# Optimization experiments

Hardware: AMD Instinct MI355X
Metric: run time of the kernel (lower is better)

The kernel has to match this reference:

```python
import jax, jax.numpy as jnp
import numpy as np
import math

B, N, C = 1, 2048, 256
H, CH = 8, 32
PQ, PV = 8, 12
CZ = 32
BQ, BK = 32, 128
NB = N // BQ
PAD = (BK - BQ) // 2
INF = 1e8
EPS = 1e-8

_KIDX = np.arange(NB)[:, None] * BQ + np.arange(BK)[None, :] - PAD
_KVALID = (_KIDX >= 0) & (_KIDX < N)
_KIDX_C = np.clip(_KIDX, 0, N - 1)


def _quat_to_rot(q):
    q = q / jnp.linalg.norm(q, axis=-1, keepdims=True)
    w, x, y, z = q[..., 0], q[..., 1], q[..., 2], q[..., 3]
    return jnp.stack([
        jnp.stack([1 - 2 * (y * y + z * z), 2 * (x * y - w * z), 2 * (x * z + w * y)], -1),
        jnp.stack([2 * (x * y + w * z), 1 - 2 * (x * x + z * z), 2 * (y * z - w * x)], -1),
        jnp.stack([2 * (x * z - w * y), 2 * (y * z + w * x), 1 - 2 * (x * x + y * y)], -1)], -2)


def _to_queries(x):
    # [B, N, ...] -> [B, NB, BQ, ...]
    return x.reshape((B, NB, BQ) + x.shape[2:])


def _to_keys(x):
    # [B, N, ...] -> [B, NB, BK, ...] zero-padded sliding key windows
    g = x[:, _KIDX_C]
    v = jnp.asarray(_KVALID, x.dtype).reshape((1, NB, BK) + (1,) * (x.ndim - 2))
    return g * v


def _ln(x):
    m = x.mean(-1, keepdims=True)
    var = x.var(-1, keepdims=True)
    return (x - m) / jnp.sqrt(var + 1e-5)


def setup_inputs():
    key = jax.random.key(0)
    ks = jax.random.split(key, 16)
    p = 0.02
    return {
        's': jax.random.normal(ks[0], (B, N, C), jnp.float32),
        'cond': jax.random.normal(ks[1], (B, N, C), jnp.float32),
        'z': jax.random.normal(ks[2], (B, NB, BQ, BK, CZ), jnp.float32),
        'trans': jax.random.normal(ks[3], (B, N, 3), jnp.float32),
        'rots': _quat_to_rot(jax.random.normal(ks[4], (B, N, 4), jnp.float32)),
        's_mask': jnp.ones((B, N), jnp.float32),
        'Wq': jax.random.normal(ks[5], (C, H * CH)) * p,
        'Wk': jax.random.normal(ks[6], (C, H * CH)) * p,
        'Wv': jax.random.normal(ks[7], (C, H * CH)) * p,
        'Wqp': jax.random.normal(ks[8], (C, H * PQ * 3)) * p,
        'Wkvp': jax.random.normal(ks[9], (C, H * (PQ + PV) * 3)) * p,
        'Wb': jax.random.normal(ks[10], (CZ, H)) * p,
        'Wdz': jax.random.normal(ks[11], (CZ, CZ // 4)) * p,
        'head_weights': jnp.full((H,), 0.5413),
        'Wout': jax.random.normal(ks[12], (H * (CZ // 4 + CH + PV * 4), C)) * p,
        'Wg': jax.random.normal(ks[13], (C, C)) * p,
        'bg': jnp.zeros((C,)),
        'Wbeta': jax.random.normal(ks[14], (C, C)) * p,
        'bbeta': jnp.zeros((C,)),
        'g_z': jnp.ones((CZ,)),
        'b_z': jnp.zeros((CZ,)),
    }


def reference(s, cond, z, trans, rots, s_mask, Wq, Wk, Wv, Wqp, Wkvp, Wb, Wdz,
              head_weights, Wout, Wg, bg, Wbeta, bbeta, g_z, b_z):
    # AdaLN on s conditioned on cond; LayerNorm on z
    s = _ln(s) * (cond @ Wg + bg) + (cond @ Wbeta + bbeta)
    z = _ln(z) * g_z + b_z

    q_in = _to_queries(s)            # [B,NB,BQ,C]
    k_in = _to_keys(s)               # [B,NB,BK,C]
    q_t = _to_queries(trans)         # [B,NB,BQ,3]
    q_R = _to_queries(rots)          # [B,NB,BQ,3,3]
    k_t = _to_keys(trans)
    k_R = _to_keys(rots)
    # zero-padded key rotations -> identity
    zero = jnp.all(k_R == 0, axis=(-2, -1))[..., None, None]
    k_R = jnp.where(zero, jnp.eye(3, dtype=k_R.dtype), k_R)

    q = (q_in @ Wq).reshape(B, NB, BQ, H, CH)
    k = (k_in @ Wk).reshape(B, NB, BK, H, CH)
    v = (k_in @ Wv).reshape(B, NB, BK, H, CH)

    q_pts = (q_in @ Wqp).reshape(B, NB, BQ, H * PQ, 3)
    q_pts = jnp.einsum('bnqij,bnqpj->bnqpi', q_R, q_pts) + q_t[..., None, :]
    q_pts = q_pts.reshape(B, NB, BQ, H, PQ, 3)

    kv_pts = (k_in @ Wkvp).reshape(B, NB, BK, H * (PQ + PV), 3)
    kv_pts = jnp.einsum('bnkij,bnkpj->bnkpi', k_R, kv_pts) + k_t[..., None, :]
    kv_pts = kv_pts.reshape(B, NB, BK, H, PQ + PV, 3)
    k_pts, v_pts = kv_pts[..., :PQ, :], kv_pts[..., PQ:, :]

    b = z @ Wb                                    # [B,NB,BQ,BK,H]
    a = jnp.einsum('bnqhc,bnkhc->bnqkh', q, k) * math.sqrt(1.0 / (3 * CH))
    a = a + math.sqrt(1.0 / 3.0) * b

    disp = q_pts[:, :, :, None] - k_pts[:, :, None]   # [B,NB,BQ,BK,H,PQ,3]
    d2 = jnp.sum(disp * disp, axis=-1)                # [B,NB,BQ,BK,H,PQ]
    hw = jax.nn.softplus(head_weights) * math.sqrt(1.0 / (3 * (PQ * 9.0 / 2)))
    pt_att = -0.5 * jnp.sum(d2 * hw[:, None], axis=-1)   # [B,NB,BQ,BK,H]

    m_q = _to_queries(s_mask[..., None])              # [B,NB,BQ,1]
    m_k = _to_keys(s_mask[..., None])                 # [B,NB,BK,1]
    attn_mask = m_q * jnp.swapaxes(m_k, -1, -2)       # [B,NB,BQ,BK]
    attn_mask = INF * (attn_mask - 1.0)

    a = a + pt_att + attn_mask[..., None]
    a = jnp.swapaxes(a, -1, -2)                       # [B,NB,BQ,H,BK]
    a = jax.nn.softmax(a, axis=-1)

    o = jnp.einsum('bnqhk,bnkhc->bnqhc', a, v).reshape(B, NB, BQ, H * CH)
    o_pt = jnp.einsum('bnqhk,bnkhvc->bnqhvc', a, v_pts)      # [B,NB,BQ,H,PV,3]
    o_pt = jnp.einsum('bnqji,bnqhvj->bnqhvi', q_R,
                      o_pt - q_t[:, :, :, None, None, :])     # invert apply
    o_pt_norm = jnp.sqrt(jnp.sum(o_pt ** 2, -1) + EPS).reshape(B, NB, BQ, H * PV)
    o_pt = o_pt.reshape(B, NB, BQ, H * PV * 3)
    pair_z = z @ Wdz                                          # [B,NB,BQ,BK,CZ//4]
    o_pair = jnp.einsum('bnqhk,bnqkc->bnqhc', a, pair_z).reshape(B, NB, BQ, H * (CZ // 4))

    out = jnp.concatenate([o, o_pt, o_pt_norm, o_pair], -1) @ Wout
    return out.reshape(B, N, C)
```

## Files before the change

kernel.cpp:

```cpp
#include <hip/hip_runtime.h>
#include <hip/hip_bf16.h>
#include <math.h>

typedef __hip_bfloat16 bf16;
typedef __attribute__((ext_vector_type(8))) short short8;
typedef __attribute__((ext_vector_type(4))) short short4v;
typedef __attribute__((ext_vector_type(4))) float f32x4;

#define NRES 2048
#define CDIM 256
#define PADK 48
#define POS 1440

static __device__ __forceinline__ float b2f(bf16 x) { return __bfloat162float(x); }
static __device__ __forceinline__ float us2f(short u) {
    return __uint_as_float(((unsigned)(unsigned short)u) << 16);
}
static __device__ __forceinline__ short f2s(float f) {
    bf16 h = __float2bfloat16(f);
    return *reinterpret_cast<short*>(&h);
}
static __device__ __forceinline__ bool flag_f32(const void* smask) {
    return *(const unsigned int*)smask == 0x3F800000u;
}
static __device__ __forceinline__ float dual_load(const void* p, size_t i, bool f32) {
    float vf = ((const float*)p)[f32 ? i : 0];
    float vb = b2f(((const bf16*)p)[f32 ? (size_t)0 : i]);
    return f32 ? vf : vb;
}

struct PrepTable {
    const void* src[8];
    bf16* dst[8];
    int srcN[8];
    int nOff[8];
    int dstStride[8];
    float scl[8];
    int tileOff[9];
    const void* s;
    const void* cond;
    bf16* condb;
    bf16* xnb;
    const void* rots;
    const void* trans;
    float* RT;
    const void* z;
    const void* Wb;
    const void* Wdz;
    const void* g_z;
    const void* b_z;
    bf16* Bzb;
    bf16* PZb;
};
__global__ __launch_bounds__(256) void k_prep(PrepTable tb, const void* __restrict__ smask) {
    __shared__ float tile[32][33];
    __shared__ float ls[8][CDIM];
    __shared__ float mrs[8][2];
    __shared__ float wb[32][8], wdz[32][8], gz[32], bz[32];
    bool f32 = flag_f32(smask);
    int b = blockIdx.x;
    int t = threadIdx.x;
    if (b < tb.tileOff[8]) {
        int s = 0;
        while (b >= tb.tileOff[s + 1]) ++s;
        int rel = b - tb.tileOff[s];
        int ntTiles = tb.srcN[s] >> 5;
        int kt = rel / ntTiles, nt = rel % ntTiles;
        const void* src = tb.src[s];
        int srcN = tb.srcN[s];
        float scl = tb.scl[s];
        int tx = t & 31, ty = t >> 5;
#pragma unroll
        for (int r = 0; r < 4; ++r) {
            int srow = kt * 32 + ty + r * 8;
            int scol = nt * 32 + tx;
            tile[ty + r * 8][tx] = dual_load(src, (size_t)srow * srcN + scol, f32);
        }
        __syncthreads();
        bf16* dst = tb.dst[s];
#pragma unroll
        for (int r = 0; r < 4; ++r) {
            int n = nt * 32 + ty + r * 8 + tb.nOff[s];
            int k = kt * 32 + tx;
            dst[(size_t)n * tb.dstStride[s] + k] = __float2bfloat16(tile[tx][ty + r * 8] * scl);
        }
        return;
    }
    b -= tb.tileOff[8];
    if (b < 256) {
        int i0 = b * 2048;
        for (int i = t; i < 2048; i += 256)
            tb.condb[i0 + i] = __float2bfloat16(dual_load(tb.cond, (size_t)(i0 + i), f32));
        return;
    }
    b -= 256;
    if (b < 256) {
        int r0 = b * 8;
        for (int i = t; i < 8 * CDIM; i += 256) {
            int r = i >> 8, c = i & 255;
            ls[r][c] = dual_load(tb.s, (size_t)(r0 + r) * CDIM + c, f32);
        }
        __syncthreads();
        int wave = t >> 6, lane = t & 63;
        for (int rr = 0; rr < 2; ++rr) {
            int r = wave * 2 + rr;
            float sum = 0.f, sq = 0.f;
            for (int j = lane; j < CDIM; j += 64) { float v = ls[r][j]; sum += v; sq += v * v; }
            for (int off = 32; off; off >>= 1) { sum += __shfl_xor(sum, off); sq += __shfl_xor(sq, off); }
            if (lane == 0) {
                float m = sum / CDIM;
                float var = fmaxf(sq / CDIM - m * m, 0.f);
                mrs[r][0] = m; mrs[r][1] = rsqrtf(var + 1e-5f);
            }
        }
        __syncthreads();
        int c = t;
#pragma unroll
        for (int r = 0; r < 8; ++r)
            tb.xnb[(size_t)(r0 + r) * CDIM + c] = __float2bfloat16((ls[r][c] - mrs[r][0]) * mrs[r][1]);
        return;
    }
    b -= 256;
    if (b < 96) {
        int i = b * 256 + t;
        int row = i / 12, c = i % 12;
        float v = (c < 9) ? dual_load(tb.rots, (size_t)row * 9 + c, f32)
                          : dual_load(tb.trans, (size_t)row * 3 + (c - 9), f32);
        tb.RT[i] = v;
        return;
    }
    b -= 96;
    {
        int j = t >> 3, c = t & 7;
        wb[j][c] = 0.5773502691896258f * dual_load(tb.Wb, t, f32);
        wdz[j][c] = dual_load(tb.Wdz, t, f32);
    }
    if (t < 32) { gz[t] = dual_load(tb.g_z, t, f32); bz[t] = dual_load(tb.b_z, t, f32); }
    __syncthreads();
    size_t r = (size_t)b * 256 + t;
    float zv[32];
    float sum = 0.f, sq = 0.f;
    if (f32) {
        const float4* zp = (const float4*)((const float*)tb.z + r * 32);
#pragma unroll
        for (int j4 = 0; j4 < 8; ++j4) {
            float4 v4 = zp[j4];
            zv[j4 * 4 + 0] = v4.x; zv[j4 * 4 + 1] = v4.y; zv[j4 * 4 + 2] = v4.z; zv[j4 * 4 + 3] = v4.w;
        }
    } else {
        const bf16* zp = (const bf16*)tb.z + r * 32;
#pragma unroll
        for (int j = 0; j < 32; ++j) zv[j] = b2f(zp[j]);
    }
#pragma unroll
    for (int j = 0; j < 32; ++j) { float v = zv[j]; sum += v; sq += v * v; }
    float m = sum / 32.f;
    float var = fmaxf(sq / 32.f - m * m, 0.f);
    float rstd = rsqrtf(var + 1e-5f);
#pragma unroll
    for (int j = 0; j < 32; ++j) zv[j] = (zv[j] - m) * rstd * gz[j] + bz[j];
    float bacc[8], pacc[8];
#pragma unroll
    for (int c = 0; c < 8; ++c) { bacc[c] = 0.f; pacc[c] = 0.f; }
    for (int j = 0; j < 32; ++j) {
        float v = zv[j];
#pragma unroll
        for (int c = 0; c < 8; ++c) { bacc[c] += v * wb[j][c]; pacc[c] += v * wdz[j][c]; }
    }
    int n = (int)(r >> 12);
    int q = (int)(r >> 7) & 31;
    int k = (int)r & 127;
#pragma unroll
    for (int h = 0; h < 8; ++h)
        tb.Bzb[(size_t)n * 32768 + (size_t)h * 4096 + q * 128 + k] = __float2bfloat16(bacc[h]);
#pragma unroll
    for (int c = 0; c < 8; ++c)
        tb.PZb[(((size_t)(n * 32 + q)) * 8 + c) * 128 + k] = __float2bfloat16(pacc[c]);
}

__global__ __launch_bounds__(256) void k_gb(
    const bf16* __restrict__ condb, const bf16* __restrict__ GWt, const bf16* __restrict__ xnb,
    const void* __restrict__ bg, const void* __restrict__ bbeta,
    const void* __restrict__ smask, bf16* __restrict__ SQb)
{
    bool f32 = flag_f32(smask);
    int wid = threadIdx.x >> 6, lane = threadIdx.x & 63;
    int tid = blockIdx.x * 4 + wid;
    int mt = tid >> 4, nt = tid & 15;
    int idx = lane & 15, quad = lane >> 4;
    const bf16* Ap = condb + (size_t)(mt * 16 + idx) * 256 + quad * 8;
    const bf16* B0 = GWt + (size_t)(nt * 16 + idx) * 256 + quad * 8;
    const bf16* B1 = GWt + (size_t)(256 + nt * 16 + idx) * 256 + quad * 8;
    f32x4 a0 = {0,0,0,0}, a1 = {0,0,0,0};
    for (int k = 0; k < 256; k += 32) {
        short8 af = *(const short8*)(Ap + k);
        a0 = __builtin_amdgcn_mfma_f32_16x16x32_bf16(af, *(const short8*)(B0 + k), a0, 0, 0, 0);
        a1 = __builtin_amdgcn_mfma_f32_16x16x32_bf16(af, *(const short8*)(B1 + k), a1, 0, 0, 0);
    }
    int ocol = nt * 16 + idx;
    float bgc = dual_load(bg, ocol, f32), bbc = dual_load(bbeta, ocol, f32);
    int orow = mt * 16 + quad * 4;
#pragma unroll
    for (int r = 0; r < 4; ++r) {
        int row = orow + r;
        float xn = b2f(xnb[(size_t)row * 256 + ocol]);
        SQb[(size_t)row * 256 + ocol] = __float2bfloat16(xn * (a0[r] + bgc) + (a1[r] + bbc));
    }
}

__global__ __launch_bounds__(256) void k_gemm22b(
    const bf16* __restrict__ A, const bf16* __restrict__ Bt, bf16* __restrict__ C,
    int N, int K, int totalWaves)
{
    int wid = threadIdx.x >> 6, lane = threadIdx.x & 63;
    int tid = blockIdx.x * 4 + wid;
    if (tid >= totalWaves) return;
    int tiles_n = N >> 5;
    int mt = tid / tiles_n, nt = tid % tiles_n;
    int idx = lane & 15, quad = lane >> 4;
    const bf16* Ap0 = A + (size_t)(mt * 32 + idx) * K + quad * 8;
    const bf16* Ap1 = Ap0 + (size_t)16 * K;
    const bf16* Bp0 = Bt + (size_t)(nt * 32 + idx) * K + quad * 8;
    const bf16* Bp1 = Bp0 + (size_t)16 * K;
    f32x4 a00 = {0,0,0,0}, a01 = {0,0,0,0}, a10 = {0,0,0,0}, a11 = {0,0,0,0};
    for (int k = 0; k < K; k += 32) {
        short8 af0 = *(const short8*)(Ap0 + k);
        short8 af1 = *(const short8*)(Ap1 + k);
        short8 bf0 = *(const short8*)(Bp0 + k);
        short8 bf1 = *(const short8*)(Bp1 + k);
        a00 = __builtin_amdgcn_mfma_f32_16x16x32_bf16(af0, bf0, a00, 0, 0, 0);
        a01 = __builtin_amdgcn_mfma_f32_16x16x32_bf16(af0, bf1, a01, 0, 0, 0);
        a10 = __builtin_amdgcn_mfma_f32_16x16x32_bf16(af1, bf0, a10, 0, 0, 0);
        a11 = __builtin_amdgcn_mfma_f32_16x16x32_bf16(af1, bf1, a11, 0, 0, 0);
    }
    int orow = mt * 32 + quad * 4;
    int ocol = nt * 32 + idx;
#pragma unroll
    for (int r = 0; r < 4; ++r) {
        C[(size_t)(orow + r) * N + ocol] = __float2bfloat16(a00[r]);
        C[(size_t)(orow + r) * N + ocol + 16] = __float2bfloat16(a01[r]);
        C[(size_t)(orow + r + 16) * N + ocol] = __float2bfloat16(a10[r]);
        C[(size_t)(orow + r + 16) * N + ocol + 16] = __float2bfloat16(a11[r]);
    }
}

__global__ __launch_bounds__(256) void k_attn_out(
    const bf16* __restrict__ POb,
    const bf16* __restrict__ Bzb, const bf16* __restrict__ PZb,
    const float* __restrict__ RT,
    const void* __restrict__ smask, const void* __restrict__ head_weights,
    bf16* __restrict__ CATb)
{
    __shared__ char buf[70016];
    __shared__ float rowq[32], rowk[128], mk[128], mqv[32];
    short* QfS = (short*)buf;
    short* KfS = (short*)(buf + 4608);
    short* VtS = (short*)(buf + 23040);
    short* AsS = (short*)(buf + 44800);
    float* S   = (float*)(buf + 53504);
    float* OPT = (float*)(buf + 53504);
    short* PtsS = (short*)(buf + 44800);
    short* QpS  = (short*)(buf + 62208);

    const int n = blockIdx.x >> 3, h = blockIdx.x & 7;
    const int t = threadIdx.x;
    const bool f32 = flag_f32(smask);
    const int n32 = n * 32;

    float hwv = dual_load(head_weights, h, f32);
    float ptc = -0.5f * log1pf(expf(hwv)) * 0.09622504486493764f;
    float m2ptc = -2.f * ptc;
    const short8 zero8 = {0,0,0,0,0,0,0,0};
    const short4v zero4 = {0,0,0,0};

    if (t < 128) {
        int q = t >> 2, g = t & 3;
        *(short8*)(QfS + q * 72 + g * 8) =
            *(const short8*)(POb + (size_t)(n32 + q) * POS + h * 32 + g * 8);
    }
    for (int i = t; i < 512; i += 256) {
        int k = i >> 2, g = i & 3;
        int kg = n32 + k - PADK;
        short8 v = zero8;
        if (kg >= 0 && kg < NRES)
            v = *(const short8*)(POb + (size_t)kg * POS + 256 + h * 32 + g * 8);
        *(short8*)(KfS + k * 72 + g * 8) = v;
    }
    for (int i = t; i < 512; i += 256) {
        int k = i >> 2, g = i & 3;
        int kg = n32 + k - PADK;
        short8 v = zero8;
        if (kg >= 0 && kg < NRES)
            v = *(const short8*)(POb + (size_t)kg * POS + 512 + h * 32 + g * 8);
#pragma unroll
        for (int j = 0; j < 8; ++j) VtS[(g * 8 + j) * 136 + k] = v[j];
    }
    for (int i = t; i < 1920; i += 256) {
        int k = i / 15, g = i % 15;
        int kg = n32 + k - PADK;
        short4v v = zero4;
        if (kg >= 0 && kg < NRES)
            v = *(const short4v*)(POb + (size_t)kg * POS + 960 + h * 60 + g * 4);
        *(short4v*)(PtsS + k * 68 + g * 4) = v;
    }
    if (t < 192) {
        int q = t / 6, g = t % 6;
        *(short4v*)(QpS + q * 28 + g * 4) =
            *(const short4v*)(POb + (size_t)(n32 + q) * POS + 768 + h * 24 + g * 4);
    }
    for (int i = t; i < 320; i += 256) {
        if (i < 64) { int q = i >> 1, g = i & 1; *(short8*)(QfS + q * 72 + 56 + g * 8) = zero8; }
        else { int j = i - 64; int k = j >> 1, g = j & 1; *(short8*)(KfS + k * 72 + 56 + g * 8) = zero8; }
    }
    for (int i = t; i < 204; i += 256) {
        int r = 68 + i / 17, sg = i % 17;
        *(short8*)(VtS + r * 136 + sg * 8) = zero8;
    }
    __syncthreads();

    {
        int k = t >> 1, half = t & 1;
        int kg = n32 + k - PADK;
        bool valid = (kg >= 0 && kg < NRES);
        if (valid) {
            const float4* rt = (const float4*)(RT + (size_t)kg * 12);
            float4 r0 = rt[0], r1 = rt[1], r2 = rt[2];
            float s2 = 0.f;
            int j0 = half * 10;
#pragma unroll
            for (int jj = 0; jj < 10; ++jj) {
                int j = j0 + jj;
                float x = us2f(PtsS[k * 68 + j * 3 + 0]);
                float y = us2f(PtsS[k * 68 + j * 3 + 1]);
                float z = us2f(PtsS[k * 68 + j * 3 + 2]);
                float p0 = r0.x * x + r0.y * y + r0.z * z + r2.y;
                float p1 = r0.w * x + r1.x * y + r1.y * z + r2.z;
                float p2 = r1.z * x + r1.w * y + r2.x * z + r2.w;
                if (j < 8) {
                    KfS[k * 72 + 32 + j * 3 + 0] = f2s(p0);
                    KfS[k * 72 + 32 + j * 3 + 1] = f2s(p1);
                    KfS[k * 72 + 32 + j * 3 + 2] = f2s(p2);
                    s2 += p0 * p0 + p1 * p1 + p2 * p2;
                } else {
                    int v = j - 8;
                    VtS[(32 + v * 3 + 0) * 136 + k] = f2s(p0);
                    VtS[(32 + v * 3 + 1) * 136 + k] = f2s(p1);
                    VtS[(32 + v * 3 + 2) * 136 + k] = f2s(p2);
                }
            }
            if (half == 0) {
                rowk[k] = ptc * s2;
                mk[k] = dual_load(smask, kg, f32);
            }
        } else {
            if (half == 0) {
                for (int c = 32; c < 56; ++c) KfS[k * 72 + c] = 0;
                for (int x = 32; x < 50; ++x) VtS[x * 136 + k] = 0;
                rowk[k] = 0.f; mk[k] = 0.f;
            } else {
                for (int x = 50; x < 68; ++x) VtS[x * 136 + k] = 0;
            }
        }
    }
    if (t < 32) {
        int q = t;
        int g = n32 + q;
        const float4* rt = (const float4*)(RT + (size_t)g * 12);
        float4 r0 = rt[0], r1 = rt[1], r2 = rt[2];
        mqv[q] = dual_load(smask, g, f32);
        float s2 = 0.f;
#pragma unroll
        for (int p = 0; p < 8; ++p) {
            float x = us2f(QpS[q * 28 + p * 3 + 0]);
            float y = us2f(QpS[q * 28 + p * 3 + 1]);
            float z = us2f(QpS[q * 28 + p * 3 + 2]);
            float p0 = r0.x * x + r0.y * y + r0.z * z + r2.y;
            float p1 = r0.w * x + r1.x * y + r1.y * z + r2.z;
            float p2 = r1.z * x + r1.w * y + r2.x * z + r2.w;
            QfS[q * 72 + 32 + p * 3 + 0] = f2s(m2ptc * p0);
            QfS[q * 72 + 32 + p * 3 + 1] = f2s(m2ptc * p1);
            QfS[q * 72 + 32 + p * 3 + 2] = f2s(m2ptc * p2);
            s2 += p0 * p0 + p1 * p1 + p2 * p2;
        }
        rowq[q] = ptc * s2;
    }
    __syncthreads();

    const int wid = t >> 6, lane = t & 63, idx = lane & 15, quad = lane >> 4;
#pragma unroll
    for (int i = 0; i < 4; ++i) {
        int tt = wid * 4 + i;
        int mt = tt >> 3, nt = tt & 7;
        f32x4 acc = {0.f, 0.f, 0.f, 0.f};
#pragma unroll
        for (int kk = 0; kk < 2; ++kk) {
            short8 af  = *(const short8*)(QfS + (mt * 16 + idx) * 72 + kk * 32 + quad * 8);
            short8 bfv = *(const short8*)(KfS + (nt * 16 + idx) * 72 + kk * 32 + quad * 8);
            acc = __builtin_amdgcn_mfma_f32_16x16x32_bf16(af, bfv, acc, 0, 0, 0);
        }
#pragma unroll
        for (int r = 0; r < 4; ++r) {
            int q = mt * 16 + quad * 4 + r;
            int k = nt * 16 + idx;
            float bz = b2f(Bzb[(size_t)n * 32768 + (size_t)h * 4096 + q * 128 + k]);
            float msk = 1e8f * (mqv[q] * mk[k] - 1.f);
            S[q * 129 + k] = acc[r] + bz + rowq[q] + rowk[k] + msk;
        }
    }
    __syncthreads();

    for (int rr = 0; rr < 8; ++rr) {
        int q = wid * 8 + rr;
        float v0 = S[q * 129 + lane], v1 = S[q * 129 + lane + 64];
        float mx = fmaxf(v0, v1);
        for (int off = 32; off; off >>= 1) mx = fmaxf(mx, __shfl_xor(mx, off));
        float e0 = expf(v0 - mx), e1 = expf(v1 - mx);
        float sm = e0 + e1;
        for (int off = 32; off; off >>= 1) sm += __shfl_xor(sm, off);
        float inv = 1.f / sm;
        AsS[q * 136 + lane] = f2s(e0 * inv);
        AsS[q * 136 + lane + 64] = f2s(e1 * inv);
    }
    __syncthreads();

    {
        int q = t >> 3, c = t & 7;
        const short8* pzp = (const short8*)(PZb + ((size_t)(n32 + q) * 8 + c) * 128);
        const short8* asp = (const short8*)(AsS + q * 136);
        float acc = 0.f;
        for (int k8 = 0; k8 < 16; ++k8) {
            short8 pv = pzp[k8];
            short8 av = asp[k8];
#pragma unroll
            for (int j = 0; j < 8; ++j) acc += us2f(av[j]) * us2f(pv[j]);
        }
        CATb[(size_t)(n32 + q) * 704 + 640 + h * 8 + c] = __float2bfloat16(acc);
    }
#pragma unroll
    for (int i = 0; i < 3; ++i) {
        int tt = wid + i * 4;
        if (tt >= 10) break;
        int mt = tt / 5, nt = tt % 5;
        f32x4 acc = {0.f, 0.f, 0.f, 0.f};
#pragma unroll
        for (int kk = 0; kk < 4; ++kk) {
            short8 af  = *(const short8*)(AsS + (mt * 16 + idx) * 136 + kk * 32 + quad * 8);
            short8 bfv = *(const short8*)(VtS + (nt * 16 + idx) * 136 + kk * 32 + quad * 8);
            acc = __builtin_amdgcn_mfma_f32_16x16x32_bf16(af, bfv, acc, 0, 0, 0);
        }
        int x = nt * 16 + idx;
#pragma unroll
        for (int r = 0; r < 4; ++r) {
            int q = mt * 16 + quad * 4 + r;
            if (x < 32)
                CATb[(size_t)(n32 + q) * 704 + h * 32 + x] = __float2bfloat16(acc[r]);
            else if (x < 68)
                OPT[q * 37 + (x - 32)] = acc[r];
        }
    }
    __syncthreads();

    for (int i = t; i < 384; i += 256) {
        int q = i / 12, v = i % 12;
        int g = n32 + q;
        const float4* rt = (const float4*)(RT + (size_t)g * 12);
        float4 r0 = rt[0], r1 = rt[1], r2 = rt[2];
        float x = OPT[q * 37 + v * 3 + 0] - r2.y;
        float y = OPT[q * 37 + v * 3 + 1] - r2.z;
        float z = OPT[q * 37 + v * 3 + 2] - r2.w;
        float o0 = r0.x * x + r0.w * y + r1.z * z;
        float o1 = r0.y * x + r1.x * y + r1.w * z;
        float o2 = r0.z * x + r1.y * y + r2.x * z;
        size_t cb = (size_t)g * 704;
        CATb[cb + 256 + (h * 12 + v) * 3 + 0] = __float2bfloat16(o0);
        CATb[cb + 256 + (h * 12 + v) * 3 + 1] = __float2bfloat16(o1);
        CATb[cb + 256 + (h * 12 + v) * 3 + 2] = __float2bfloat16(o2);
        CATb[cb + 544 + h * 12 + v] = __float2bfloat16(sqrtf(o0 * o0 + o1 * o1 + o2 * o2 + 1e-8f));
    }
}

__global__ __launch_bounds__(256) void k_gemm(
    const bf16* __restrict__ A, const bf16* __restrict__ Bt, void* __restrict__ Cv,
    int N, int K, int totalTiles, const void* __restrict__ smask)
{
    int wid = threadIdx.x >> 6, lane = threadIdx.x & 63;
    int tid = blockIdx.x * 4 + wid;
    if (tid >= totalTiles) return;
    int tiles_n = N >> 4;
    int mt = tid / tiles_n, nt = tid % tiles_n;
    int idx = lane & 15, quad = lane >> 4;
    const bf16* Ap = A + (size_t)(mt * 16 + idx) * K + quad * 8;
    const bf16* Bp = Bt + (size_t)(nt * 16 + idx) * K + quad * 8;
    f32x4 acc = {0.f, 0.f, 0.f, 0.f};
    for (int k = 0; k < K; k += 32) {
        short8 af = *(const short8*)(Ap + k);
        short8 bfv = *(const short8*)(Bp + k);
        acc = __builtin_amdgcn_mfma_f32_16x16x32_bf16(af, bfv, acc, 0, 0, 0);
    }
    int orow = mt * 16 + quad * 4;
    int ocol = nt * 16 + idx;
    if (flag_f32(smask)) {
        float* C = (float*)Cv;
#pragma unroll
        for (int r = 0; r < 4; ++r) C[(size_t)(orow + r) * N + ocol] = acc[r];
    } else {
        bf16* C = (bf16*)Cv;
#pragma unroll
        for (int r = 0; r < 4; ++r) C[(size_t)(orow + r) * N + ocol] = __float2bfloat16(acc[r]);
    }
}

extern "C" void kernel_launch(void* const* d_in, const int* in_sizes, int n_in,
                              void* d_out, int out_size, void* d_ws, size_t ws_size,
                              hipStream_t stream) {
    const void* s       = d_in[0];
    const void* cond    = d_in[1];
    const void* z       = d_in[2];
    const void* trans   = d_in[3];
    const void* rots    = d_in[4];
    const void* s_mask  = d_in[5];
    const void* Wq      = d_in[6];
    const void* Wk      = d_in[7];
    const void* Wv      = d_in[8];
    const void* Wqp     = d_in[9];
    const void* Wkvp    = d_in[10];
    const void* Wb      = d_in[11];
    const void* Wdz     = d_in[12];
    const void* hweights= d_in[13];
    const void* Wout    = d_in[14];
    const void* Wg      = d_in[15];
    const void* bg      = d_in[16];
    const void* Wbeta   = d_in[17];
    const void* bbeta   = d_in[18];
    const void* g_z     = d_in[19];
    const void* b_z     = d_in[20];

    float* ws = (float*)d_ws;
    bf16* POb   = (bf16*)(ws);
    bf16* Bzb   = (bf16*)(ws + 1474560);
    bf16* PZb   = (bf16*)(ws + 2523136);
    bf16* SQb   = (bf16*)(ws + 3571712);
    bf16* condb = (bf16*)(ws + 3833856);
    bf16* xnb   = (bf16*)(ws + 4096000);
    bf16* CATb  = (bf16*)(ws + 4358144);
    bf16* PWt   = (bf16*)(ws + 5079040);
    bf16* GWt   = (bf16*)(ws + 5263360);
    bf16* FWt   = (bf16*)(ws + 5328896);
    float* RT   = (float*)(ws + 5419008);

    PrepTable tb;
    const float qkscale = 0.10206207261596575f;
    tb.src[0] = Wq;   tb.dst[0] = PWt; tb.srcN[0] = 256; tb.nOff[0] = 0;   tb.dstStride[0] = 256; tb.scl[0] = qkscale;
    tb.src[1] = Wk;   tb.dst[1] = PWt; tb.srcN[1] = 256; tb.nOff[1] = 256; tb.dstStride[1] = 256; tb.scl[1] = 1.f;
    tb.src[2] = Wv;   tb.dst[2] = PWt; tb.srcN[2] = 256; tb.nOff[2] = 512; tb.dstStride[2] = 256; tb.scl[2] = 1.f;
    tb.src[3] = Wqp;  tb.dst[3] = PWt; tb.srcN[3] = 192; tb.nOff[3] = 768; tb.dstStride[3] = 256; tb.scl[3] = 1.f;
    tb.src[4] = Wkvp; tb.dst[4] = PWt; tb.srcN[4] = 480; tb.nOff[4] = 960; tb.dstStride[4] = 256; tb.scl[4] = 1.f;
    tb.src[5] = Wg;   tb.dst[5] = GWt; tb.srcN[5] = 256; tb.nOff[5] = 0;   tb.dstStride[5] = 256; tb.scl[5] = 1.f;
    tb.src[6] = Wbeta;tb.dst[6] = GWt; tb.srcN[6] = 256; tb.nOff[6] = 256; tb.dstStride[6] = 256; tb.scl[6] = 1.f;
    tb.src[7] = Wout; tb.dst[7] = FWt; tb.srcN[7] = 256; tb.nOff[7] = 0;   tb.dstStride[7] = 704; tb.scl[7] = 1.f;
    int tc[8] = {64, 64, 64, 48, 120, 64, 64, 176};
    tb.tileOff[0] = 0;
    for (int i = 0; i < 8; ++i) tb.tileOff[i + 1] = tb.tileOff[i] + tc[i];
    tb.s = s; tb.cond = cond; tb.condb = condb; tb.xnb = xnb;
    tb.rots = rots; tb.trans = trans; tb.RT = RT;
    tb.z = z; tb.Wb = Wb; tb.Wdz = Wdz; tb.g_z = g_z; tb.b_z = b_z;
    tb.Bzb = Bzb; tb.PZb = PZb;

    dim3 blk(256);
    k_prep<<<dim3(2296), blk, 0, stream>>>(tb, s_mask);
    k_gb<<<dim3(512), blk, 0, stream>>>(condb, GWt, xnb, bg, bbeta, s_mask, SQb);
    k_gemm22b<<<dim3(720), blk, 0, stream>>>(SQb, PWt, POb, 1440, 256, 2880);
    k_attn_out<<<dim3(512), blk, 0, stream>>>(POb, Bzb, PZb, RT, s_mask, hweights, CATb);
    k_gemm<<<dim3(512), blk, 0, stream>>>(CATb, FWt, d_out, 256, 704, 2048, s_mask);
}
```

Baseline: 177.5 us.

## Prefetch frames, Bz tile and pair-z into registers/LDS; reorder prep blocks

In the attention kernel, rotation/translation frames and masks are loaded into registers at kernel start, and the per-head Bz bias tile is staged into LDS with vector loads instead of scattered global reads inside the score loop. The PZb rows are loaded into registers before the V MFMA so their latency overlaps it, and the o_pair dot product runs afterwards. In the prep kernel the heavy z-layernorm blocks are moved to the front of the grid so they are scheduled first. This adds about 8.7KB of LDS and 64 registers of short8 per thread, which may reduce occupancy.

```diff
diff --git a/kernel.cpp b/kernel.cpp
--- a/kernel.cpp
+++ b/kernel.cpp
@@ -60,6 +60,56 @@
     bool f32 = flag_f32(smask);
     int b = blockIdx.x;
     int t = threadIdx.x;
+    if (b < 1024) {
+        {
+            int j = t >> 3, c = t & 7;
+            wb[j][c] = 0.5773502691896258f * dual_load(tb.Wb, t, f32);
+            wdz[j][c] = dual_load(tb.Wdz, t, f32);
+        }
+        if (t < 32) { gz[t] = dual_load(tb.g_z, t, f32); bz[t] = dual_load(tb.b_z, t, f32); }
+        __syncthreads();
+        size_t r = (size_t)b * 256 + t;
+        float zv[32];
+        float sum = 0.f, sq = 0.f;
+        if (f32) {
+            const float4* zp = (const float4*)((const float*)tb.z + r * 32);
+#pragma unroll
+            for (int j4 = 0; j4 < 8; ++j4) {
+                float4 v4 = zp[j4];
+                zv[j4 * 4 + 0] = v4.x; zv[j4 * 4 + 1] = v4.y; zv[j4 * 4 + 2] = v4.z; zv[j4 * 4 + 3] = v4.w;
+            }
+        } else {
+            const bf16* zp = (const bf16*)tb.z + r * 32;
+#pragma unroll
+            for (int j = 0; j < 32; ++j) zv[j] = b2f(zp[j]);
+        }
+#pragma unroll
+        for (int j = 0; j < 32; ++j) { float v = zv[j]; sum += v; sq += v * v; }
+        float m = sum / 32.f;
+        float var = fmaxf(sq / 32.f - m * m, 0.f);
+        float rstd = rsqrtf(var + 1e-5f);
+#pragma unroll
+        for (int j = 0; j < 32; ++j) zv[j] = (zv[j] - m) * rstd * gz[j] + bz[j];
+        float bacc[8], pacc[8];
+#pragma unroll
+        for (int c = 0; c < 8; ++c) { bacc[c] = 0.f; pacc[c] = 0.f; }
+        for (int j = 0; j < 32; ++j) {
+            float v = zv[j];
+#pragma unroll
+            for (int c = 0; c < 8; ++c) { bacc[c] += v * wb[j][c]; pacc[c] += v * wdz[j][c]; }
+        }
+        int n = (int)(r >> 12);
+        int q = (int)(r >> 7) & 31;
+        int k = (int)r & 127;
+#pragma unroll
+        for (int h = 0; h < 8; ++h)
+            tb.Bzb[(size_t)n * 32768 + (size_t)h * 4096 + q * 128 + k] = __float2bfloat16(bacc[h]);
+#pragma unroll
+        for (int c = 0; c < 8; ++c)
+            tb.PZb[(((size_t)(n * 32 + q)) * 8 + c) * 128 + k] = __float2bfloat16(pacc[c]);
+        return;
+    }
+    b -= 1024;
     if (b < tb.tileOff[8]) {
         int s = 0;
         while (b >= tb.tileOff[s + 1]) ++s;
@@ -121,61 +171,11 @@
         return;
     }
     b -= 256;
-    if (b < 96) {
-        int i = b * 256 + t;
-        int row = i / 12, c = i % 12;
-        float v = (c < 9) ? dual_load(tb.rots, (size_t)row * 9 + c, f32)
-                          : dual_load(tb.trans, (size_t)row * 3 + (c - 9), f32);
-        tb.RT[i] = v;
-        return;
-    }
-    b -= 96;
-    {
-        int j = t >> 3, c = t & 7;
-        wb[j][c] = 0.5773502691896258f * dual_load(tb.Wb, t, f32);
-        wdz[j][c] = dual_load(tb.Wdz, t, f32);
-    }
-    if (t < 32) { gz[t] = dual_load(tb.g_z, t, f32); bz[t] = dual_load(tb.b_z, t, f32); }
-    __syncthreads();
-    size_t r = (size_t)b * 256 + t;
-    float zv[32];
-    float sum = 0.f, sq = 0.f;
-    if (f32) {
-        const float4* zp = (const float4*)((const float*)tb.z + r * 32);
-#pragma unroll
-        for (int j4 = 0; j4 < 8; ++j4) {
-            float4 v4 = zp[j4];
-            zv[j4 * 4 + 0] = v4.x; zv[j4 * 4 + 1] = v4.y; zv[j4 * 4 + 2] = v4.z; zv[j4 * 4 + 3] = v4.w;
-        }
-    } else {
-        const bf16* zp = (const bf16*)tb.z + r * 32;
-#pragma unroll
-        for (int j = 0; j < 32; ++j) zv[j] = b2f(zp[j]);
-    }
-#pragma unroll
-    for (int j = 0; j < 32; ++j) { float v = zv[j]; sum += v; sq += v * v; }
-    float m = sum / 32.f;
-    float var = fmaxf(sq / 32.f - m * m, 0.f);
-    float rstd = rsqrtf(var + 1e-5f);
-#pragma unroll
-    for (int j = 0; j < 32; ++j) zv[j] = (zv[j] - m) * rstd * gz[j] + bz[j];
-    float bacc[8], pacc[8];
-#pragma unroll
-    for (int c = 0; c < 8; ++c) { bacc[c] = 0.f; pacc[c] = 0.f; }
-    for (int j = 0; j < 32; ++j) {
-        float v = zv[j];
-#pragma unroll
-        for (int c = 0; c < 8; ++c) { bacc[c] += v * wb[j][c]; pacc[c] += v * wdz[j][c]; }
-    }
-    int n = (int)(r >> 12);
-    int q = (int)(r >> 7) & 31;
-    int k = (int)r & 127;
-#pragma unroll
-    for (int h = 0; h < 8; ++h)
-        tb.Bzb[(size_t)n * 32768 + (size_t)h * 4096 + q * 128 + k] = __float2bfloat16(bacc[h]);
-#pragma unroll
-    for (int c = 0; c < 8; ++c)
-        tb.PZb[(((size_t)(n * 32 + q)) * 8 + c) * 128 + k] = __float2bfloat16(pacc[c]);
+    int i = b * 256 + t;
+    int row = i / 12, c = i % 12;
+    float v = (c < 9) ? dual_load(tb.rots, (size_t)row * 9 + c, f32)
+                      : dual_load(tb.trans, (size_t)row * 3 + (c - 9), f32);
+    tb.RT[i] = v;
 }
 
 __global__ __launch_bounds__(256) void k_gb(
@@ -251,7 +251,7 @@
     const void* __restrict__ smask, const void* __restrict__ head_weights,
     bf16* __restrict__ CATb)
 {
-    __shared__ char buf[70016];
+    __shared__ char buf[78720];
     __shared__ float rowq[32], rowk[128], mk[128], mqv[32];
     short* QfS = (short*)buf;
     short* KfS = (short*)(buf + 4608);
@@ -259,6 +259,7 @@
     short* AsS = (short*)(buf + 44800);
     float* S   = (float*)(buf + 53504);
     float* OPT = (float*)(buf + 53504);
+    short* BzS = (short*)(buf + 70016);
     short* PtsS = (short*)(buf + 44800);
     short* QpS  = (short*)(buf + 62208);
 
@@ -272,6 +273,24 @@
     float m2ptc = -2.f * ptc;
     const short8 zero8 = {0,0,0,0,0,0,0,0};
     const short4v zero4 = {0,0,0,0};
+
+    const int kR = t >> 1, halfR = t & 1;
+    const int kgR = n32 + kR - PADK;
+    const bool validR = (kgR >= 0 && kgR < NRES);
+    float4 kr0, kr1, kr2;
+    float kmv = 0.f;
+    if (validR) {
+        const float4* rt = (const float4*)(RT + (size_t)kgR * 12);
+        kr0 = rt[0]; kr1 = rt[1]; kr2 = rt[2];
+        if (halfR == 0) kmv = dual_load(smask, kgR, f32);
+    }
+    float4 qr0, qr1, qr2;
+    float qmv = 0.f;
+    if (t < 32) {
+        const float4* rt = (const float4*)(RT + (size_t)(n32 + t) * 12);
+        qr0 = rt[0]; qr1 = rt[1]; qr2 = rt[2];
+        qmv = dual_load(smask, n32 + t, f32);
+    }
 
     if (t < 128) {
         int q = t >> 2, g = t & 3;
@@ -295,6 +314,13 @@
 #pragma unroll
         for (int j = 0; j < 8; ++j) VtS[(g * 8 + j) * 136 + k] = v[j];
     }
+    {
+        const short8* bsrc = (const short8*)(Bzb + (size_t)n * 32768 + (size_t)h * 4096);
+        for (int i = t; i < 512; i += 256) {
+            int row = i >> 4, g = i & 15;
+            *(short8*)(BzS + row * 136 + g * 8) = bsrc[i];
+        }
+    }
     for (int i = t; i < 1920; i += 256) {
         int k = i / 15, g = i % 15;
         int kg = n32 + k - PADK;
@@ -319,64 +345,56 @@
     __syncthreads();
 
     {
-        int k = t >> 1, half = t & 1;
-        int kg = n32 + k - PADK;
-        bool valid = (kg >= 0 && kg < NRES);
-        if (valid) {
-            const float4* rt = (const float4*)(RT + (size_t)kg * 12);
-            float4 r0 = rt[0], r1 = rt[1], r2 = rt[2];
+        if (validR) {
             float s2 = 0.f;
-            int j0 = half * 10;
+            int j0 = halfR * 10;
 #pragma unroll
             for (int jj = 0; jj < 10; ++jj) {
                 int j = j0 + jj;
-                float x = us2f(PtsS[k * 68 + j * 3 + 0]);
-                float y = us2f(PtsS[k * 68 + j * 3 + 1]);
-                float z = us2f(PtsS[k * 68 + j * 3 + 2]);
-                float p0 = r0.x * x + r0.y * y + r0.z * z + r2.y;
-                float p1 = r0.w * x + r1.x * y + r1.y * z + r2.z;
-                float p2 = r1.z * x + r1.w * y + r2.x * z + r2.w;
+                float x = us2f(PtsS[kR * 68 + j * 3 + 0]);
+                float y = us2f(PtsS[kR * 68 + j * 3 + 1]);
+                float z = us2f(PtsS[kR * 68 + j * 3 + 2]);
+                float p0 = kr0.x * x + kr0.y * y + kr0.z * z + kr2.y;
+                float p1 = kr0.w * x + kr1.x * y + kr1.y * z + kr2.z;
+                float p2 = kr1.z * x + kr1.w * y + kr2.x * z + kr2.w;
                 if (j < 8) {
-                    KfS[k * 72 + 32 + j * 3 + 0] = f2s(p0);
-                    KfS[k * 72 + 32 + j * 3 + 1] = f2s(p1);
-                    KfS[k * 72 + 32 + j * 3 + 2] = f2s(p2);
+                    KfS[kR * 72 + 32 + j * 3 + 0] = f2s(p0);
+                    KfS[kR * 72 + 32 + j * 3 + 1] = f2s(p1);
+                    KfS[kR * 72 + 32 + j * 3 + 2] = f2s(p2);
                     s2 += p0 * p0 + p1 * p1 + p2 * p2;
                 } else {
                     int v = j - 8;
-                    VtS[(32 + v * 3 + 0) * 136 + k] = f2s(p0);
-                    VtS[(32 + v * 3 + 1) * 136 + k] = f2s(p1);
-                    VtS[(32 + v * 3 + 2) * 136 + k] = f2s(p2);
+                    VtS[(32 + v * 3 + 0) * 136 + kR] = f2s(p0);
+                    VtS[(32 + v * 3 + 1) * 136 + kR] = f2s(p1);
+                    VtS[(32 + v * 3 + 2) * 136 + kR] = f2s(p2);
                 }
             }
-            if (half == 0) {
-                rowk[k] = ptc * s2;
-                mk[k] = dual_load(smask, kg, f32);
+            if (halfR == 0) {
+                rowk[kR] = ptc * s2;
+                mk[kR] = kmv;
             }
         } else {
-            if (half == 0) {
-                for (int c = 32; c < 56; ++c) KfS[k * 72 + c] = 0;
-                for (int x = 32; x < 50; ++x) VtS[x * 136 + k] = 0;
-                rowk[k] = 0.f; mk[k] = 0.f;
+            if (halfR == 0) {
+                for (int c = 32; c < 56; ++c) KfS[kR * 72 + c] = 0;
+                for (int x = 32; x < 50; ++x) VtS[x * 136 + kR] = 0;
+                rowk[kR] = 0.f; mk[kR] = 0.f;
             } else {
-                for (int x = 50; x < 68; ++x) VtS[x * 136 + k] = 0;
+                for (int x = 50; x < 68; ++x) VtS[x * 136 + kR] = 0;
             }
         }
     }
     if (t < 32) {
         int q = t;
-        int g = n32 + q;
-        const float4* rt = (const float4*)(RT + (size_t)g * 12);
-        float4 r0 = rt[0], r1 = rt[1], r2 = rt[2];
-        mqv[q] = dual_load(smask, g, f32);
+        mqv[q] = qmv;
         float s2 = 0.f;
 #pragma unroll
         for (int p = 0; p < 8; ++p) {
             float x = us2f(QpS[q * 28 + p * 3 + 0]);
             float y = us2f(QpS[q * 28 + p * 3 + 1]);
             float z = us2f(QpS[q * 28 + p * 3 + 2]);
-            float p0 = r0.x * x + r0.y * y + r0.z * z + r2.y;
-            float p1 = r0.w * x + r1.x * y + r1.y * z + r2.z;
-            float p2 = r1.z * x + r1.w * y + r2.x * z + r2.w;
+            float p0 = qr0.x * x + qr0.y * y + qr0.z * z + qr2.y;
+            float p1 = qr0.w * x + qr1.x * y + qr1.y * z + qr2.z;
+            float p2 = qr1.z * x + qr1.w * y + qr2.x * z + qr2.w;
             QfS[q * 72 + 32 + p * 3 + 0] = f2s(m2ptc * p0);
             QfS[q * 72 + 32 + p * 3 + 1] = f2s(m2ptc * p1);
             QfS[q * 72 + 32 + p * 3 + 2] = f2s(m2ptc * p2);
@@ -402,7 +420,7 @@
         for (int r = 0; r < 4; ++r) {
             int q = mt * 16 + quad * 4 + r;
             int k = nt * 16 + idx;
-            float bz = b2f(Bzb[(size_t)n * 32768 + (size_t)h * 4096 + q * 128 + k]);
+            float bz = us2f(BzS[q * 136 + k]);
             float msk = 1e8f * (mqv[q] * mk[k] - 1.f);
             S[q * 129 + k] = acc[r] + bz + rowq[q] + rowk[k] + msk;
         }
@@ -423,18 +441,12 @@
     }
     __syncthreads();
 
+    short8 pzr[16];
     {
         int q = t >> 3, c = t & 7;
         const short8* pzp = (const short8*)(PZb + ((size_t)(n32 + q) * 8 + c) * 128);
-        const short8* asp = (const short8*)(AsS + q * 136);
-        float acc = 0.f;
-        for (int k8 = 0; k8 < 16; ++k8) {
-            short8 pv = pzp[k8];
-            short8 av = asp[k8];
-#pragma unroll
-            for (int j = 0; j < 8; ++j) acc += us2f(av[j]) * us2f(pv[j]);
-        }
-        CATb[(size_t)(n32 + q) * 704 + 640 + h * 8 + c] = __float2bfloat16(acc);
+#pragma unroll
+        for (int k8 = 0; k8 < 16; ++k8) pzr[k8] = pzp[k8];
     }
 #pragma unroll
     for (int i = 0; i < 3; ++i) {
@@ -457,6 +469,18 @@
             else if (x < 68)
                 OPT[q * 37 + (x - 32)] = acc[r];
         }
+    }
+    {
+        int q = t >> 3, c = t & 7;
+        const short8* asp = (const short8*)(AsS + q * 136);
+        float acc = 0.f;
+        for (int k8 = 0; k8 < 16; ++k8) {
+            short8 pv = pzr[k8];
+            short8 av = asp[k8];
+#pragma unroll
+            for (int j = 0; j < 8; ++j) acc += us2f(av[j]) * us2f(pv[j]);
+        }
+        CATb[(size_t)(n32 + q) * 704 + 640 + h * 8 + c] = __float2bfloat16(acc);
     }
     __syncthreads();
 
```

Result: no change. 175.4 us (-1.2%).
